# Optimization experiments

Hardware: AMD Instinct MI355X
Metric: run time of the kernel (lower is better)

Reference implementation:

```python
import jax, jax.numpy as jnp
import numpy as np


def setup_inputs() -> dict:
    B, n, emb, K = 8, 128, 256, 8
    N = B * n            # total nodes
    Eg = n               # edges per graph (one out-edge per node)
    E = B * Eg           # total edges
    E2 = E * K           # total edge-to-edge edges
    key = jax.random.key(0)
    k1, k2, k3, k4 = jax.random.split(key, 4)
    x = jax.random.normal(k1, (N, emb), jnp.float32)
    edge_attr = jax.random.normal(k2, (E, emb), jnp.float32)
    enc_W = jax.random.normal(k3, (3, emb), jnp.float32)
    e2e_W = jax.random.normal(k4, (3, emb), jnp.float32)
    # deterministic simple-graph edges: node i -> node (i+1) mod n within each graph
    e = np.arange(E); g = e // Eg; el = e % Eg
    src = g * n + el
    dst = g * n + (el + 1) % n
    edge_index = jnp.asarray(np.stack([src, dst]), jnp.int32)
    batch_vec = jnp.asarray(np.arange(N) // n, jnp.int32)
    # e2e graph: edge-node s connected to edge-nodes (s+1..s+K) mod Eg within graph
    f = np.arange(E2); fg = f // (Eg * K); fl = f % (Eg * K)
    s_e = fl % Eg; d_e = (s_e + 1 + fl // Eg) % Eg
    e2e_edge_index = jnp.asarray(np.stack([fg * Eg + s_e, fg * Eg + d_e]), jnp.int32)
    e_batch = jnp.asarray(np.arange(E) // Eg, jnp.int32)
    # each e2e edge carries features of the dst node of its source edge
    e2e_node_index = jnp.asarray(dst[fg * Eg + s_e], jnp.int32)
    return {"x": x, "edge_attr": edge_attr, "enc_W": enc_W, "e2e_W": e2e_W,
            "edge_index": edge_index, "batch_vec": batch_vec,
            "e2e_edge_index": e2e_edge_index, "e_batch": e_batch,
            "e2e_node_index": e2e_node_index, "n_graphs": B}


def _offsets(bvec, B):
    # start offset of each graph in the packed (node or edge) dimension
    counts = jax.ops.segment_sum(jnp.ones_like(bvec), bvec, num_segments=B)
    return jnp.concatenate([jnp.zeros((1,), counts.dtype), jnp.cumsum(counts)[:-1]])


def reference(x, edge_attr, enc_W, e2e_W, edge_index, batch_vec,
              e2e_edge_index, e_batch, e2e_node_index, n_graphs):
    B = int(n_graphs)
    N, emb = x.shape
    n = N // B
    E = edge_attr.shape[0]
    Eg = E // B
    mask = jnp.array([0.0, 1.0, 1.0], x.dtype)[:, None]  # Embedding padding_idx=0

    # ---- node-level dense edge features ----
    node_off = _offsets(batch_vec, B)
    src, dst = edge_index[0], edge_index[1]
    g = batch_vec[src]
    li = src - node_off[g]
    lj = dst - node_off[g]
    ea = edge_attr + x[src] + x[dst]                       # [E, emb]
    edge_dense = jnp.zeros((B, n, n, emb), x.dtype).at[g, li, lj].add(ea)
    # edge type codes: 0 = connected, 1 = diagonal, 2 = disconnected
    adj = jnp.zeros((B, n, n), jnp.int32).at[g, li, lj].add(2)
    lall = jnp.arange(N) - node_off[batch_vec]
    adj = adj.at[batch_vec, lall, lall].add(1)
    edge_dense = edge_dense + (enc_W * mask)[2 - adj]

    # ---- edge-to-edge dense features ----
    x2 = x + jax.ops.segment_sum(edge_attr, dst, num_segments=N)
    e_off = _offsets(e_batch, B)
    es, ed = e2e_edge_index[0], e2e_edge_index[1]
    eg = e_batch[es]
    eli = es - e_off[eg]
    elj = ed - e_off[eg]
    e2e_dense = jnp.zeros((B, Eg, Eg, emb), x.dtype).at[eg, eli, elj].add(x2[e2e_node_index])
    adj2 = jnp.zeros((B, Eg, Eg), jnp.int32).at[eg, eli, elj].add(2)
    leall = jnp.arange(E) - e_off[e_batch]
    adj2 = adj2.at[e_batch, leall, leall].add(1)
    e2e_dense = e2e_dense + (e2e_W * mask)[2 - adj2]

    return edge_dense, e2e_dense
```

## Files before the change

kernel.cpp:

```cpp
#include <hip/hip_runtime.h>

#define MAXB 1024

__global__ void offsets_k(const int* __restrict__ bv, int N,
                          const int* __restrict__ eb, int E,
                          const int* __restrict__ nG,
                          int* __restrict__ node_off, int* __restrict__ e_off) {
    __shared__ int c1[MAXB];
    __shared__ int c2[MAXB];
    int B = nG[0];
    if (B > MAXB) B = MAXB;
    for (int i = threadIdx.x; i < B; i += blockDim.x) { c1[i] = 0; c2[i] = 0; }
    __syncthreads();
    for (int i = threadIdx.x; i < N; i += blockDim.x) atomicAdd(&c1[bv[i]], 1);
    for (int i = threadIdx.x; i < E; i += blockDim.x) atomicAdd(&c2[eb[i]], 1);
    __syncthreads();
    if (threadIdx.x == 0) {
        int a = 0, b = 0;
        for (int g = 0; g < B; ++g) {
            node_off[g] = a; a += c1[g];
            e_off[g]    = b; b += c2[g];
        }
    }
}

__global__ void x2_copy_k(const float4* __restrict__ x, float4* __restrict__ x2, int n4) {
    int t = blockIdx.x * blockDim.x + threadIdx.x;
    if (t < n4) x2[t] = x[t];
}

__global__ void x2_add_k(const float* __restrict__ edge_attr,
                         const int* __restrict__ edge_index,
                         int E, int emb, float* __restrict__ x2) {
    int t = blockIdx.x * blockDim.x + threadIdx.x;
    if (t >= E * emb) return;
    int e = t / emb;
    int c = t - e * emb;
    int dst = edge_index[E + e];
    atomicAdd(&x2[dst * emb + c], edge_attr[t]);
}

__global__ void fill_k(float4* __restrict__ out, unsigned int total4,
                       const float4* __restrict__ encW,
                       const float4* __restrict__ e2eW,
                       const int* __restrict__ nG,
                       int N, int E, int emb4) {
    int B = nG[0];
    unsigned int n  = (unsigned int)(N / B);
    unsigned int Eg = (unsigned int)(E / B);
    unsigned int uemb4 = (unsigned int)emb4;
    unsigned int edge4 = (unsigned int)N * n * uemb4;
    unsigned int stride = gridDim.x * blockDim.x;
    for (unsigned int idx = blockIdx.x * blockDim.x + threadIdx.x; idx < total4; idx += stride) {
        unsigned int r = idx;
        const float4* W = encW;
        unsigned int dim = n;
        if (r >= edge4) { r -= edge4; W = e2eW; dim = Eg; }
        unsigned int cell = r / uemb4;
        unsigned int c4 = r - cell * uemb4;
        unsigned int j = cell % dim;
        unsigned int i = (cell / dim) % dim;
        out[idx] = (i == j) ? W[uemb4 + c4] : W[2u * uemb4 + c4];
    }
}

__global__ void scatter_edge_k(const float4* __restrict__ edge_attr,
                               const float4* __restrict__ x,
                               const int* __restrict__ edge_index,
                               const int* __restrict__ bv,
                               const int* __restrict__ node_off,
                               const float4* __restrict__ encW,
                               const int* __restrict__ nG,
                               int N, int E, int emb4,
                               float4* __restrict__ out) {
    int t = blockIdx.x * blockDim.x + threadIdx.x;
    if (t >= E * emb4) return;
    int e = t / emb4;
    int c4 = t - e * emb4;
    int src = edge_index[e];
    int dst = edge_index[E + e];
    int g = bv[src];
    int B = nG[0];
    int n = N / B;
    int li = src - node_off[g];
    int lj = dst - node_off[g];
    float4 a  = edge_attr[t];
    float4 xs = x[(long)src * emb4 + c4];
    float4 xd = x[(long)dst * emb4 + c4];
    float4 v;
    v.x = a.x + xs.x + xd.x;
    v.y = a.y + xs.y + xd.y;
    v.z = a.z + xs.z + xd.z;
    v.w = a.w + xs.w + xd.w;
    if (li == lj) {
        float4 wv = encW[2 * emb4 + c4];
        v.x += wv.x; v.y += wv.y; v.z += wv.z; v.w += wv.w;
    }
    long addr = ((long)(g * n + li) * n + lj) * emb4 + c4;
    out[addr] = v;
}

__global__ void scatter_e2e_k(const float* __restrict__ x2f,
                              const int* __restrict__ e2e_ei,
                              const int* __restrict__ eb,
                              const int* __restrict__ e_off,
                              const int* __restrict__ e2e_nidx,
                              const float4* __restrict__ e2eW,
                              const int* __restrict__ nG,
                              int N, int E, int E2, int emb4,
                              float4* __restrict__ out) {
    int t = blockIdx.x * blockDim.x + threadIdx.x;
    if (t >= E2 * emb4) return;
    int f = t / emb4;
    int c4 = t - f * emb4;
    int es = e2e_ei[f];
    int ed = e2e_ei[E2 + f];
    int g = eb[es];
    int B = nG[0];
    int n = N / B;
    int Eg = E / B;
    int eli = es - e_off[g];
    int elj = ed - e_off[g];
    const float4* x2 = (const float4*)x2f;
    float4 v = x2[(long)e2e_nidx[f] * emb4 + c4];
    if (eli == elj) {
        float4 wv = e2eW[2 * emb4 + c4];
        v.x += wv.x; v.y += wv.y; v.z += wv.z; v.w += wv.w;
    }
    long edge4 = (long)N * n * emb4;
    long addr = edge4 + ((long)(g * Eg + eli) * Eg + elj) * emb4 + c4;
    out[addr] = v;
}

extern "C" void kernel_launch(void* const* d_in, const int* in_sizes, int n_in,
                              void* d_out, int out_size, void* d_ws, size_t ws_size,
                              hipStream_t stream) {
    const float* x          = (const float*)d_in[0];
    const float* edge_attr  = (const float*)d_in[1];
    const float* enc_W      = (const float*)d_in[2];
    const float* e2e_W      = (const float*)d_in[3];
    const int* edge_index   = (const int*)d_in[4];
    const int* batch_vec    = (const int*)d_in[5];
    const int* e2e_ei       = (const int*)d_in[6];
    const int* e_batch      = (const int*)d_in[7];
    const int* e2e_nidx     = (const int*)d_in[8];
    const int* nG           = (const int*)d_in[9];

    int emb  = in_sizes[2] / 3;
    int emb4 = emb / 4;
    int N    = in_sizes[0] / emb;
    int E    = in_sizes[1] / emb;
    int E2   = in_sizes[8];

    char* ws      = (char*)d_ws;
    int* node_off = (int*)ws;
    int* e_off    = (int*)(ws + 4096);
    float* x2     = (float*)(ws + 8192);

    offsets_k<<<1, 256, 0, stream>>>(batch_vec, N, e_batch, E, nG, node_off, e_off);

    int n4x = (N * emb) / 4;
    x2_copy_k<<<(n4x + 255) / 256, 256, 0, stream>>>((const float4*)x, (float4*)x2, n4x);

    int tadd = E * emb;
    x2_add_k<<<(tadd + 255) / 256, 256, 0, stream>>>(edge_attr, edge_index, E, emb, x2);

    unsigned int total4 = (unsigned int)(out_size / 4);
    fill_k<<<8192, 256, 0, stream>>>((float4*)d_out, total4,
                                     (const float4*)enc_W, (const float4*)e2e_W,
                                     nG, N, E, emb4);

    int t1 = E * emb4;
    scatter_edge_k<<<(t1 + 255) / 256, 256, 0, stream>>>(
        (const float4*)edge_attr, (const float4*)x, edge_index, batch_vec,
        node_off, (const float4*)enc_W, nG, N, E, emb4, (float4*)d_out);

    int t2 = E2 * emb4;
    scatter_e2e_k<<<(t2 + 255) / 256, 256, 0, stream>>>(
        x2, e2e_ei, e_batch, e_off, e2e_nidx,
        (const float4*)e2e_W, nG, N, E, E2, emb4, (float4*)d_out);
}
```

Baseline: 290.6 us.

## Restructure fill kernel per-cell with nontemporal stores and merge prep kernels

The fill kernel is restructured so each wave handles four cells: 16 lanes per cell compute the diagonal test once and loop over the embedding with nontemporal vector stores. This replaces per-element division and modulo in a grid-stride loop and aims to reduce cache pollution on the large output write. The offsets and x2 copy kernels are merged into one launch, with block 0 also computing offsets, to save a launch. The total output is about 1.1 GB of writes, so the fill is bandwidth-bound and the gain depends on whether nontemporal stores raise effective write bandwidth.

```diff
diff --git a/kernel.cpp b/kernel.cpp
--- a/kernel.cpp
+++ b/kernel.cpp
@@ -2,31 +2,33 @@
 
 #define MAXB 1024
 
-__global__ void offsets_k(const int* __restrict__ bv, int N,
-                          const int* __restrict__ eb, int E,
-                          const int* __restrict__ nG,
-                          int* __restrict__ node_off, int* __restrict__ e_off) {
-    __shared__ int c1[MAXB];
-    __shared__ int c2[MAXB];
-    int B = nG[0];
-    if (B > MAXB) B = MAXB;
-    for (int i = threadIdx.x; i < B; i += blockDim.x) { c1[i] = 0; c2[i] = 0; }
-    __syncthreads();
-    for (int i = threadIdx.x; i < N; i += blockDim.x) atomicAdd(&c1[bv[i]], 1);
-    for (int i = threadIdx.x; i < E; i += blockDim.x) atomicAdd(&c2[eb[i]], 1);
-    __syncthreads();
-    if (threadIdx.x == 0) {
-        int a = 0, b = 0;
-        for (int g = 0; g < B; ++g) {
-            node_off[g] = a; a += c1[g];
-            e_off[g]    = b; b += c2[g];
+typedef float fx4 __attribute__((ext_vector_type(4)));
+
+__global__ void prep_k(const float4* __restrict__ x, float4* __restrict__ x2, int n4,
+                       const int* __restrict__ bv, int N,
+                       const int* __restrict__ eb, int E,
+                       const int* __restrict__ nG,
+                       int* __restrict__ node_off, int* __restrict__ e_off) {
+    int t = blockIdx.x * blockDim.x + threadIdx.x;
+    if (t < n4) x2[t] = x[t];
+    if (blockIdx.x == 0) {
+        __shared__ int c1[MAXB];
+        __shared__ int c2[MAXB];
+        int B = nG[0];
+        if (B > MAXB) B = MAXB;
+        for (int i = threadIdx.x; i < B; i += blockDim.x) { c1[i] = 0; c2[i] = 0; }
+        __syncthreads();
+        for (int i = threadIdx.x; i < N; i += blockDim.x) atomicAdd(&c1[bv[i]], 1);
+        for (int i = threadIdx.x; i < E; i += blockDim.x) atomicAdd(&c2[eb[i]], 1);
+        __syncthreads();
+        if (threadIdx.x == 0) {
+            int a = 0, b = 0;
+            for (int g = 0; g < B; ++g) {
+                node_off[g] = a; a += c1[g];
+                e_off[g]    = b; b += c2[g];
+            }
         }
     }
-}
-
-__global__ void x2_copy_k(const float4* __restrict__ x, float4* __restrict__ x2, int n4) {
-    int t = blockIdx.x * blockDim.x + threadIdx.x;
-    if (t < n4) x2[t] = x[t];
 }
 
 __global__ void x2_add_k(const float* __restrict__ edge_attr,
@@ -40,27 +42,33 @@
     atomicAdd(&x2[dst * emb + c], edge_attr[t]);
 }
 
-__global__ void fill_k(float4* __restrict__ out, unsigned int total4,
-                       const float4* __restrict__ encW,
-                       const float4* __restrict__ e2eW,
-                       const int* __restrict__ nG,
-                       int N, int E, int emb4) {
+__global__ void fill2_k(fx4* __restrict__ out,
+                        const fx4* __restrict__ encW,
+                        const fx4* __restrict__ e2eW,
+                        const int* __restrict__ nG,
+                        int N, int E, int emb4, unsigned int total_cells) {
     int B = nG[0];
     unsigned int n  = (unsigned int)(N / B);
     unsigned int Eg = (unsigned int)(E / B);
-    unsigned int uemb4 = (unsigned int)emb4;
-    unsigned int edge4 = (unsigned int)N * n * uemb4;
-    unsigned int stride = gridDim.x * blockDim.x;
-    for (unsigned int idx = blockIdx.x * blockDim.x + threadIdx.x; idx < total4; idx += stride) {
-        unsigned int r = idx;
-        const float4* W = encW;
-        unsigned int dim = n;
-        if (r >= edge4) { r -= edge4; W = e2eW; dim = Eg; }
-        unsigned int cell = r / uemb4;
-        unsigned int c4 = r - cell * uemb4;
-        unsigned int j = cell % dim;
-        unsigned int i = (cell / dim) % dim;
-        out[idx] = (i == j) ? W[uemb4 + c4] : W[2u * uemb4 + c4];
+    unsigned int cells1 = (unsigned int)N * n;
+    unsigned int tid  = blockIdx.x * blockDim.x + threadIdx.x;
+    unsigned int wave = tid >> 6;
+    unsigned int lane = tid & 63u;
+    unsigned int s = lane >> 4;
+    unsigned int c = lane & 15u;
+    unsigned int cell = wave * 4u + s;
+    if (cell >= total_cells) return;
+    unsigned int r = cell;
+    const fx4* W = encW;
+    unsigned int dim = n;
+    if (r >= cells1) { r -= cells1; W = e2eW; dim = Eg; }
+    unsigned int within = r % (dim * dim);
+    bool diag = (within % (dim + 1u)) == 0u;
+    const fx4* Wrow = W + (size_t)(diag ? emb4 : 2 * emb4);
+    fx4* cellout = out + (size_t)cell * emb4;
+    for (unsigned int k = c; k < (unsigned int)emb4; k += 16u) {
+        fx4 v = Wrow[k];
+        __builtin_nontemporal_store(v, &cellout[k]);
     }
 }
 
@@ -157,18 +165,22 @@
     int* e_off    = (int*)(ws + 4096);
     float* x2     = (float*)(ws + 8192);
 
-    offsets_k<<<1, 256, 0, stream>>>(batch_vec, N, e_batch, E, nG, node_off, e_off);
-
     int n4x = (N * emb) / 4;
-    x2_copy_k<<<(n4x + 255) / 256, 256, 0, stream>>>((const float4*)x, (float4*)x2, n4x);
+    int prep_blocks = (n4x + 255) / 256;
+    if (prep_blocks < 1) prep_blocks = 1;
+    prep_k<<<prep_blocks, 256, 0, stream>>>((const float4*)x, (float4*)x2, n4x,
+                                            batch_vec, N, e_batch, E, nG,
+                                            node_off, e_off);
 
     int tadd = E * emb;
     x2_add_k<<<(tadd + 255) / 256, 256, 0, stream>>>(edge_attr, edge_index, E, emb, x2);
 
-    unsigned int total4 = (unsigned int)(out_size / 4);
-    fill_k<<<8192, 256, 0, stream>>>((float4*)d_out, total4,
-                                     (const float4*)enc_W, (const float4*)e2e_W,
-                                     nG, N, E, emb4);
+    unsigned int total_cells = (unsigned int)(out_size / emb);
+    unsigned int waves = (total_cells + 3u) / 4u;
+    unsigned int fill_blocks = (waves + 3u) / 4u;
+    fill2_k<<<fill_blocks, 256, 0, stream>>>((fx4*)d_out,
+                                             (const fx4*)enc_W, (const fx4*)e2e_W,
+                                             nG, N, E, emb4, total_cells);
 
     int t1 = E * emb4;
     scatter_edge_k<<<(t1 + 255) / 256, 256, 0, stream>>>(
```

Result: slower. 299.8 us (+3.2%).
